# Kernel tuning notes

Hardware: AMD Instinct MI355X
Metric: run time of the kernel (lower is better)

Reference implementation:

```python
import jax, jax.numpy as jnp
import numpy as np

B, C, H, W = 64, 3, 256, 256
K = 2  # multi_n_num
EPS_NORM = 1e-8
EPS_DEN = 1e-7
SCALE = 0.01


def setup_inputs() -> dict:
    key = jax.random.key(0)
    ka, kp, kn, kj = jax.random.split(key, 4)
    a = jax.random.normal(ka, (B, C, H, W), dtype=jnp.float32)
    p = jax.random.normal(kp, (B, C, H, W), dtype=jnp.float32)
    n = jax.random.normal(kn, (B, C, H, W), dtype=jnp.float32)
    # sample_with_j(B, 2, i) -> [i, random j != i]
    ar = jnp.arange(B, dtype=jnp.int64)
    off = jax.random.randint(kj, (B,), 1, B)  # offset in [1, B) guarantees j != i
    neg_idx = jnp.stack([ar, (ar + off) % B], axis=1).astype(jnp.int64)  # [B, K]
    return {"a": a, "p": p, "n": n, "neg_idx": neg_idx}


def _fft_norm(x):
    # torch.fft.fft2 over last two dims -> complex, same rank as x
    f = jnp.fft.fft2(x, axes=(-2, -1))  # [B, C, H, W] complex64
    # torch.norm(f, p=2, dim=1, keepdim=True) on complex = sqrt(sum |f|^2 over C)
    nrm = jnp.sqrt(jnp.sum(jnp.abs(f) ** 2, axis=1, keepdims=True))
    return f / (nrm + EPS_NORM) * SCALE


def reference(a, p, n, neg_idx):
    af = _fft_norm(a)
    pf = _fft_norm(p)
    nf = _fft_norm(n)
    # L1Loss on complex tensors = mean |diff| (complex magnitude)
    d_ap = jnp.mean(jnp.abs(af - pf), axis=(1, 2, 3))  # [B]
    n_sel = nf[neg_idx]  # [B, K, C, H, W]
    d_an = jnp.mean(jnp.abs(af[:, None] - n_sel), axis=(2, 3, 4))  # [B, K]
    contrastive = jnp.sum(d_ap[:, None] / (d_an + EPS_DEN))
    return contrastive / (K * B)
```

## Files before the change

### kernel.cpp

```cpp
#include <hip/hip_runtime.h>
#include <hip/hip_fp16.h>

#define B_ 64
#define SW_ 132
#define SIMG_ (256 * SW_)
#define TIMG_ (3 * SIMG_)
#define TELEMS_ ((size_t)B_ * TIMG_)
#define SST_ 257

__device__ __forceinline__ float2 cmul(float2 a, float2 b) {
  return make_float2(a.x * b.x - a.y * b.y, a.x * b.y + a.y * b.x);
}
__device__ __forceinline__ unsigned f2u(float2 v) {
  __half2 h = __float22half2_rn(v);
  return __builtin_bit_cast(unsigned, h);
}
__device__ __forceinline__ float2 u2f(unsigned u) {
  return __half22float2(__builtin_bit_cast(__half2, u));
}

__device__ __forceinline__ void bfly4(float2 x[4], float2 ta, float2 tb, float2 tc, bool tw) {
  float2 a = make_float2(x[0].x + x[2].x, x[0].y + x[2].y);
  float2 b = make_float2(x[0].x - x[2].x, x[0].y - x[2].y);
  float2 c = make_float2(x[1].x + x[3].x, x[1].y + x[3].y);
  float2 d = make_float2(x[1].x - x[3].x, x[1].y - x[3].y);
  float2 y1 = make_float2(b.x + d.y, b.y - d.x);
  float2 y2 = make_float2(a.x - c.x, a.y - c.y);
  float2 y3 = make_float2(b.x - d.y, b.y + d.x);
  x[0] = make_float2(a.x + c.x, a.y + c.y);
  if (tw) { y1 = cmul(y1, ta); y2 = cmul(y2, tb); y3 = cmul(y3, tc); }
  x[1] = y1; x[2] = y2; x[3] = y3;
}

__device__ __forceinline__ void xbit(unsigned& A, unsigned& B, int bit, int r) {
  bool hi = (r >> bit) & 1;
  int send = hi ? (int)A : (int)B;
  int got = __shfl_xor(send, 1 << bit, 64);
  if (hi) A = (unsigned)got; else B = (unsigned)got;
}
__device__ __forceinline__ void xdigit(unsigned u[4], int bit, int r) {
  xbit(u[0], u[1], bit, r);
  xbit(u[2], u[3], bit, r);
  xbit(u[0], u[2], bit + 1, r);
  xbit(u[1], u[3], bit + 1, r);
}

__device__ __forceinline__ void fft256_reg(float2 x[4], unsigned u[4], int r,
                                           const float2 tw[9]) {
  bfly4(x, tw[0], tw[1], tw[2], true);
#pragma unroll
  for (int s = 0; s < 4; ++s) u[s] = f2u(x[s]);
  xdigit(u, 4, r);
#pragma unroll
  for (int s = 0; s < 4; ++s) x[s] = u2f(u[s]);
  bfly4(x, tw[3], tw[4], tw[5], true);
#pragma unroll
  for (int s = 0; s < 4; ++s) u[s] = f2u(x[s]);
  xdigit(u, 2, r);
#pragma unroll
  for (int s = 0; s < 4; ++s) x[s] = u2f(u[s]);
  bfly4(x, tw[6], tw[7], tw[8], true);
#pragma unroll
  for (int s = 0; s < 4; ++s) u[s] = f2u(x[s]);
  xdigit(u, 0, r);
#pragma unroll
  for (int s = 0; s < 4; ++s) x[s] = u2f(u[s]);
  bfly4(x, tw[0], tw[0], tw[0], false);
#pragma unroll
  for (int s = 0; s < 4; ++s) u[s] = f2u(x[s]);
}

__global__ __launch_bounds__(1024, 4) void fft2_fused(const float* __restrict__ a,
                                                      const float* __restrict__ p,
                                                      const float* __restrict__ n,
                                                      unsigned* __restrict__ outbase) {
  __shared__ unsigned S[129 * SST_];

  int tid = threadIdx.x;
  int wv = tid >> 6;
  int r = tid & 63;
  int tensor = blockIdx.x / 192;
  int plane = blockIdx.x % 192;
  const float* in = (tensor == 0 ? a : (tensor == 1 ? p : n)) + (size_t)plane * 65536;
  unsigned* outp = outbase + (size_t)tensor * TELEMS_ + (size_t)plane * SIMG_;

  float2 tw[9];
  {
    float s, c;
    __sincosf(-6.283185307179586f * (float)r / 256.0f, &s, &c);
    tw[0] = make_float2(c, s); tw[1] = cmul(tw[0], tw[0]); tw[2] = cmul(tw[1], tw[0]);
    __sincosf(-6.283185307179586f * (float)(r & 15) / 64.0f, &s, &c);
    tw[3] = make_float2(c, s); tw[4] = cmul(tw[3], tw[3]); tw[5] = cmul(tw[4], tw[3]);
    __sincosf(-6.283185307179586f * (float)(r & 3) / 16.0f, &s, &c);
    tw[6] = make_float2(c, s); tw[7] = cmul(tw[6], tw[6]); tw[8] = cmul(tw[7], tw[6]);
  }
  int m = ((r & 3) << 4) | (((r >> 2) & 3) << 2) | (r >> 4);
  int mp = (64 - m) & 63;
  int rp = ((mp >> 4) & 3) | (((mp >> 2) & 3) << 2) | ((mp & 3) << 4);

  for (int it = 0; it < 8; ++it) {
    int q = it * 16 + wv;
    const float* r0 = in + (size_t)(2 * q) * 256;
    float2 x[4]; unsigned u[4];
#pragma unroll
    for (int j = 0; j < 4; ++j)
      x[j] = make_float2(r0[r + 64 * j], r0[256 + r + 64 * j]);
    fft256_reg(x, u, r, tw);
    unsigned mir[4];
#pragma unroll
    for (int t = 0; t < 4; ++t) mir[t] = (unsigned)__shfl((int)u[t], rp, 64);
#pragma unroll
    for (int s = 0; s < 2; ++s) {
      int k = 64 * s + m;
      int sp = (m == 0) ? ((4 - s) & 3) : (3 - s);
      float2 Zk = u2f(u[s]), Zm = u2f(mir[sp]);
      float2 A  = make_float2(0.5f * (Zk.x + Zm.x), 0.5f * (Zk.y - Zm.y));
      float2 Bv = make_float2(0.5f * (Zk.y + Zm.y), 0.5f * (Zm.x - Zk.x));
      S[k * SST_ + 2 * q]     = f2u(A);
      S[k * SST_ + 2 * q + 1] = f2u(Bv);
    }
    if (r == 0) {
      float2 Zk = u2f(u[2]);
      S[128 * SST_ + 2 * q]     = f2u(make_float2(Zk.x, 0.0f));
      S[128 * SST_ + 2 * q + 1] = f2u(make_float2(Zk.y, 0.0f));
    }
  }

  __syncthreads();

  for (int it = 0; it < 9; ++it) {
    int c = it * 16 + wv;
    if (c <= 128) {
      unsigned* srow = S + c * SST_;
      float2 x[4]; unsigned u[4];
#pragma unroll
      for (int j = 0; j < 4; ++j) x[j] = u2f(srow[r + 64 * j]);
      fft256_reg(x, u, r, tw);
      *(uint4*)(outp + (size_t)c * 256 + 4 * r) = make_uint4(u[0], u[1], u[2], u[3]);
    }
  }
  if (wv >= 13) {
    int c = 129 + (wv - 13);
    *(uint4*)(outp + (size_t)c * 256 + 4 * r) = make_uint4(0, 0, 0, 0);
  }
}

__device__ __forceinline__ float cab2(float2 v) { return v.x * v.x + v.y * v.y; }

__global__ __launch_bounds__(256) void dist_kernel(const unsigned* __restrict__ af,
                                                   const unsigned* __restrict__ pf,
                                                   const unsigned* __restrict__ nf,
                                                   const int* __restrict__ neg,
                                                   float* __restrict__ acc) {
  int b = blockIdx.y;
  int j = (neg[1] == 0) ? (int)((const long long*)neg)[b * 2 + 1] : neg[b * 2 + 1];
  size_t ab = (size_t)b * TIMG_;
  size_t jb = (size_t)j * TIMG_;
  int t4 = blockIdx.x * 256 + threadIdx.x;
  int flat0 = t4 * 4;
  int k2 = flat0 >> 8;
  float w = (k2 == 0 || k2 >= 128) ? 1.0f : 2.0f;

  unsigned A[3][4], P[3][4], N[3][4], M[3][4];
#pragma unroll
  for (int ch = 0; ch < 3; ++ch) {
    uint4 t;
    t = *(const uint4*)(af + ab + ch * SIMG_ + flat0); A[ch][0]=t.x; A[ch][1]=t.y; A[ch][2]=t.z; A[ch][3]=t.w;
    t = *(const uint4*)(pf + ab + ch * SIMG_ + flat0); P[ch][0]=t.x; P[ch][1]=t.y; P[ch][2]=t.z; P[ch][3]=t.w;
    t = *(const uint4*)(nf + ab + ch * SIMG_ + flat0); N[ch][0]=t.x; N[ch][1]=t.y; N[ch][2]=t.z; N[ch][3]=t.w;
    t = *(const uint4*)(nf + jb + ch * SIMG_ + flat0); M[ch][0]=t.x; M[ch][1]=t.y; M[ch][2]=t.z; M[ch][3]=t.w;
  }
  float s_ap = 0.0f, s_a0 = 0.0f, s_a1 = 0.0f;
#pragma unroll
  for (int e = 0; e < 4; ++e) {
    float2 a0 = u2f(A[0][e]), a1 = u2f(A[1][e]), a2 = u2f(A[2][e]);
    float2 p0 = u2f(P[0][e]), p1 = u2f(P[1][e]), p2 = u2f(P[2][e]);
    float2 n0 = u2f(N[0][e]), n1 = u2f(N[1][e]), n2 = u2f(N[2][e]);
    float2 m0 = u2f(M[0][e]), m1 = u2f(M[1][e]), m2 = u2f(M[2][e]);
    float sa = 0.01f / (sqrtf(cab2(a0) + cab2(a1) + cab2(a2)) + 1e-8f);
    float sp = 0.01f / (sqrtf(cab2(p0) + cab2(p1) + cab2(p2)) + 1e-8f);
    float sn = 0.01f / (sqrtf(cab2(n0) + cab2(n1) + cab2(n2)) + 1e-8f);
    float sm = 0.01f / (sqrtf(cab2(m0) + cab2(m1) + cab2(m2)) + 1e-8f);
    float dx, dy;
    dx = a0.x * sa - p0.x * sp; dy = a0.y * sa - p0.y * sp; s_ap += sqrtf(dx * dx + dy * dy);
    dx = a1.x * sa - p1.x * sp; dy = a1.y * sa - p1.y * sp; s_ap += sqrtf(dx * dx + dy * dy);
    dx = a2.x * sa - p2.x * sp; dy = a2.y * sa - p2.y * sp; s_ap += sqrtf(dx * dx + dy * dy);
    dx = a0.x * sa - n0.x * sn; dy = a0.y * sa - n0.y * sn; s_a0 += sqrtf(dx * dx + dy * dy);
    dx = a1.x * sa - n1.x * sn; dy = a1.y * sa - n1.y * sn; s_a0 += sqrtf(dx * dx + dy * dy);
    dx = a2.x * sa - n2.x * sn; dy = a2.y * sa - n2.y * sn; s_a0 += sqrtf(dx * dx + dy * dy);
    dx = a0.x * sa - m0.x * sm; dy = a0.y * sa - m0.y * sm; s_a1 += sqrtf(dx * dx + dy * dy);
    dx = a1.x * sa - m1.x * sm; dy = a1.y * sa - m1.y * sm; s_a1 += sqrtf(dx * dx + dy * dy);
    dx = a2.x * sa - m2.x * sm; dy = a2.y * sa - m2.y * sm; s_a1 += sqrtf(dx * dx + dy * dy);
  }
  s_ap *= w; s_a0 *= w; s_a1 *= w;
#pragma unroll
  for (int off = 32; off > 0; off >>= 1) {
    s_ap += __shfl_down(s_ap, off);
    s_a0 += __shfl_down(s_a0, off);
    s_a1 += __shfl_down(s_a1, off);
  }
  __shared__ float red[3][4];
  int lane = threadIdx.x & 63, wid = threadIdx.x >> 6;
  if (lane == 0) { red[0][wid] = s_ap; red[1][wid] = s_a0; red[2][wid] = s_a1; }
  __syncthreads();
  if (threadIdx.x == 0) {
    atomicAdd(&acc[b * 3 + 0], red[0][0] + red[0][1] + red[0][2] + red[0][3]);
    atomicAdd(&acc[b * 3 + 1], red[1][0] + red[1][1] + red[1][2] + red[1][3]);
    atomicAdd(&acc[b * 3 + 2], red[2][0] + red[2][1] + red[2][2] + red[2][3]);
  }
}

__global__ void zero_acc(float* acc) { acc[threadIdx.x] = 0.0f; }

__global__ void final_kernel(const float* __restrict__ acc, float* __restrict__ out) {
  int b = threadIdx.x;
  const float inv = 1.0f / 196608.0f;
  float dap = acc[b * 3 + 0] * inv;
  float da0 = acc[b * 3 + 1] * inv;
  float da1 = acc[b * 3 + 2] * inv;
  float term = dap / (da0 + 1e-7f) + dap / (da1 + 1e-7f);
#pragma unroll
  for (int off = 32; off > 0; off >>= 1) term += __shfl_down(term, off);
  if (b == 0) out[0] = term * (1.0f / 128.0f);
}

extern "C" void kernel_launch(void* const* d_in, const int* in_sizes, int n_in,
                              void* d_out, int out_size, void* d_ws, size_t ws_size,
                              hipStream_t stream) {
  const float* a = (const float*)d_in[0];
  const float* p = (const float*)d_in[1];
  const float* n = (const float*)d_in[2];
  const int* neg = (const int*)d_in[3];
  float* out = (float*)d_out;

  unsigned* base = (unsigned*)d_ws;
  float* acc = (float*)(base + 3 * TELEMS_);

  zero_acc<<<1, 192, 0, stream>>>(acc);
  fft2_fused<<<576, 1024, 0, stream>>>(a, p, n, base);
  dist_kernel<<<dim3(33, 64), 256, 0, stream>>>(base, base + TELEMS_,
                                                base + 2 * TELEMS_, neg, acc);
  final_kernel<<<1, 64, 0, stream>>>(acc, out);
}
```

Baseline: 247.0 us.

## Store FFT intermediate in fp8 shared memory with packed Nyquist column and swizzle

The intermediate row-FFT results in shared memory are now stored as fp8 pairs instead of fp16, with a skewed (rotated) index swizzle replacing the padded stride. The Nyquist column is packed into the DC column's imaginary slot, so only 128 column FFTs are run, and the DC/Nyquist pair is split afterwards. Smaller LDS use lets occupancy rise (launch bounds 1024,8). The risk is a large precision loss from fp8 quantization of spectral values, which may break accuracy tolerance.

```diff
diff --git a/kernel.cpp b/kernel.cpp
--- a/kernel.cpp
+++ b/kernel.cpp
@@ -6,7 +6,6 @@
 #define SIMG_ (256 * SW_)
 #define TIMG_ (3 * SIMG_)
 #define TELEMS_ ((size_t)B_ * TIMG_)
-#define SST_ 257
 
 __device__ __forceinline__ float2 cmul(float2 a, float2 b) {
   return make_float2(a.x * b.x - a.y * b.y, a.x * b.y + a.y * b.x);
@@ -17,6 +16,14 @@
 }
 __device__ __forceinline__ float2 u2f(unsigned u) {
   return __half22float2(__builtin_bit_cast(__half2, u));
+}
+template <bool HI>
+__device__ __forceinline__ unsigned pk8(float2 v, unsigned old) {
+  return (unsigned)__builtin_amdgcn_cvt_pk_fp8_f32(v.x, v.y, (int)old, HI);
+}
+__device__ __forceinline__ float2 up8(unsigned v) {
+  return make_float2(__builtin_amdgcn_cvt_f32_fp8((int)v, 0),
+                     __builtin_amdgcn_cvt_f32_fp8((int)v, 1));
 }
 
 __device__ __forceinline__ void bfly4(float2 x[4], float2 ta, float2 tb, float2 tc, bool tw) {
@@ -70,11 +77,11 @@
   for (int s = 0; s < 4; ++s) u[s] = f2u(x[s]);
 }
 
-__global__ __launch_bounds__(1024, 4) void fft2_fused(const float* __restrict__ a,
+__global__ __launch_bounds__(1024, 8) void fft2_fused(const float* __restrict__ a,
                                                       const float* __restrict__ p,
                                                       const float* __restrict__ n,
                                                       unsigned* __restrict__ outbase) {
-  __shared__ unsigned S[129 * SST_];
+  __shared__ unsigned S32[128 * 128];
 
   int tid = threadIdx.x;
   int wv = tid >> 6;
@@ -109,34 +116,50 @@
     unsigned mir[4];
 #pragma unroll
     for (int t = 0; t < 4; ++t) mir[t] = (unsigned)__shfl((int)u[t], rp, 64);
+    float2 ZN = u2f(u[2]);
 #pragma unroll
     for (int s = 0; s < 2; ++s) {
       int k = 64 * s + m;
       int sp = (m == 0) ? ((4 - s) & 3) : (3 - s);
       float2 Zk = u2f(u[s]), Zm = u2f(mir[sp]);
-      float2 A  = make_float2(0.5f * (Zk.x + Zm.x), 0.5f * (Zk.y - Zm.y));
-      float2 Bv = make_float2(0.5f * (Zk.y + Zm.y), 0.5f * (Zm.x - Zk.x));
-      S[k * SST_ + 2 * q]     = f2u(A);
-      S[k * SST_ + 2 * q + 1] = f2u(Bv);
+      bool pr = (m == 0) && (s == 0);
+      float2 A  = make_float2(0.5f * (Zk.x + Zm.x), pr ? ZN.x : 0.5f * (Zk.y - Zm.y));
+      float2 Bv = make_float2(0.5f * (Zk.y + Zm.y), pr ? ZN.y : 0.5f * (Zm.x - Zk.x));
+      unsigned w32 = pk8<false>(A, 0u);
+      w32 = pk8<true>(Bv, w32);
+      S32[k * 128 + ((q + k) & 127)] = w32;
     }
-    if (r == 0) {
-      float2 Zk = u2f(u[2]);
-      S[128 * SST_ + 2 * q]     = f2u(make_float2(Zk.x, 0.0f));
-      S[128 * SST_ + 2 * q + 1] = f2u(make_float2(Zk.y, 0.0f));
+  }
+
+  __syncthreads();
+
+  for (int it = 0; it < 8; ++it) {
+    int ell = it * 16 + wv;
+    const unsigned short* Sh = (const unsigned short*)S32;
+    float2 x[4]; unsigned u[4];
+#pragma unroll
+    for (int j = 0; j < 4; ++j) {
+      int c = r + 64 * j;
+      int e = ((((c >> 1) + ell) & 127) << 1) | (c & 1);
+      x[j] = up8((unsigned)Sh[ell * 256 + e]);
     }
-  }
-
-  __syncthreads();
-
-  for (int it = 0; it < 9; ++it) {
-    int c = it * 16 + wv;
-    if (c <= 128) {
-      unsigned* srow = S + c * SST_;
-      float2 x[4]; unsigned u[4];
-#pragma unroll
-      for (int j = 0; j < 4; ++j) x[j] = u2f(srow[r + 64 * j]);
-      fft256_reg(x, u, r, tw);
-      *(uint4*)(outp + (size_t)c * 256 + 4 * r) = make_uint4(u[0], u[1], u[2], u[3]);
+    fft256_reg(x, u, r, tw);
+    if (ell == 0) {
+      unsigned mir[4];
+#pragma unroll
+      for (int t = 0; t < 4; ++t) mir[t] = (unsigned)__shfl((int)u[t], rp, 64);
+      unsigned f0[4], f1[4];
+#pragma unroll
+      for (int s = 0; s < 4; ++s) {
+        int sp = (m == 0) ? ((4 - s) & 3) : (3 - s);
+        float2 Zk = u2f(u[s]), Zm = u2f(mir[sp]);
+        f0[s] = f2u(make_float2(0.5f * (Zk.x + Zm.x), 0.5f * (Zk.y - Zm.y)));
+        f1[s] = f2u(make_float2(0.5f * (Zk.y + Zm.y), 0.5f * (Zm.x - Zk.x)));
+      }
+      *(uint4*)(outp + 4 * r) = make_uint4(f0[0], f0[1], f0[2], f0[3]);
+      *(uint4*)(outp + (size_t)128 * 256 + 4 * r) = make_uint4(f1[0], f1[1], f1[2], f1[3]);
+    } else {
+      *(uint4*)(outp + (size_t)ell * 256 + 4 * r) = make_uint4(u[0], u[1], u[2], u[3]);
     }
   }
   if (wv >= 13) {
```

Measured after the change: 268.1 us. 8.5% more time.
